# Optimization experiments

Hardware: AMD Instinct MI355X
Metric: run time of the kernel (lower is better)

Reference implementation:

```python
import jax, jax.numpy as jnp
import numpy as np

LOW_DIM, SKIP_DIM, OUT_DIM = 512, 256, 256
EPS_IDW = 1e-8
EPS_LN = 1e-5
K = 3


def setup_inputs() -> dict:
    key = jax.random.key(0)
    ks = jax.random.split(key, 10)
    B, N, S = 4, 8192, 2048
    xyz_hi = jax.random.uniform(ks[0], (B, N, 3), dtype=jnp.float32)
    xyz_lo = jax.random.uniform(ks[1], (B, S, 3), dtype=jnp.float32)
    feat_skip = jax.random.normal(ks[2], (B, N, SKIP_DIM), dtype=jnp.float32)
    feat_lo = jax.random.normal(ks[3], (B, S, LOW_DIM), dtype=jnp.float32)
    in_dim = LOW_DIM + SKIP_DIM
    W1 = jax.random.normal(ks[4], (in_dim, OUT_DIM), dtype=jnp.float32) / np.sqrt(in_dim)
    b1 = jnp.zeros((OUT_DIM,), dtype=jnp.float32)
    W2 = jax.random.normal(ks[5], (OUT_DIM, OUT_DIM), dtype=jnp.float32) / np.sqrt(OUT_DIM)
    b2 = jnp.zeros((OUT_DIM,), dtype=jnp.float32)
    gamma = jnp.ones((OUT_DIM,), dtype=jnp.float32)
    beta = jnp.zeros((OUT_DIM,), dtype=jnp.float32)
    return {"xyz_hi": xyz_hi, "xyz_lo": xyz_lo, "feat_skip": feat_skip,
            "feat_lo": feat_lo, "W1": W1, "b1": b1, "W2": W2, "b2": b2,
            "gamma": gamma, "beta": beta}


def _layer_norm(x, gamma, beta):
    mu = jnp.mean(x, axis=-1, keepdims=True)
    var = jnp.mean(jnp.square(x - mu), axis=-1, keepdims=True)
    return (x - mu) * jax.lax.rsqrt(var + EPS_LN) * gamma + beta


def reference(xyz_hi, xyz_lo, feat_skip, feat_lo, W1, b1, W2, b2, gamma, beta):
    B, N, _ = xyz_hi.shape
    _, S, _ = xyz_lo.shape
    if S == 1:
        interpolated = jnp.broadcast_to(feat_lo, (B, N, feat_lo.shape[-1]))
    else:
        # pairwise Euclidean distances: (B, N, S)
        d2 = (jnp.sum(xyz_hi ** 2, -1)[:, :, None]
              + jnp.sum(xyz_lo ** 2, -1)[:, None, :]
              - 2.0 * jnp.einsum('bnd,bsd->bns', xyz_hi, xyz_lo))
        dists = jnp.sqrt(jnp.maximum(d2, 0.0))
        # smallest-3 via top_k on negated distances
        neg_d, knn_idx = jax.lax.top_k(-dists, K)          # (B, N, 3)
        dk = -neg_d
        inv_d = 1.0 / (dk + EPS_IDW)
        weights = inv_d / jnp.sum(inv_d, axis=-1, keepdims=True)  # (B, N, 3)
        # gather neighbor features: (B, N, 3, low_dim)
        knn_feat = feat_lo[jnp.arange(B)[:, None, None], knn_idx]
        interpolated = jnp.einsum('bnk,bnkc->bnc', weights, knn_feat)
    fused = jnp.concatenate([feat_skip, interpolated], axis=-1)   # (B, N, skip+low)
    h = jax.nn.relu(fused @ W1 + b1)
    h = h @ W2 + b2
    return _layer_norm(h, gamma, beta)
```

## Files before the change

kernel.cpp:

```cpp
#include <hip/hip_runtime.h>
#include <hip/hip_bf16.h>
#include <stdint.h>

typedef unsigned short u16;
typedef __attribute__((ext_vector_type(8))) short short8;
typedef __attribute__((ext_vector_type(4))) float f32x4;

#define BB 4
#define NN 8192
#define SS 2048
#define MTOT 32768
#define CSKIP 256
#define CLO 512
#define CIN 768
#define COUT 256

__device__ __forceinline__ u16 f2bf(float f) {
  unsigned u = __float_as_uint(f);
  u += 0x7fffu + ((u >> 16) & 1u);
  return (u16)(u >> 16);
}

__device__ __forceinline__ void gl_lds16(const void* g, void* l) {
  __builtin_amdgcn_global_load_lds(
      (const __attribute__((address_space(1))) void*)g,
      (__attribute__((address_space(3))) void*)l, 16, 0, 0);
}

__global__ __launch_bounds__(256) void wconv_kernel(const float* __restrict__ W1,
                                                    const float* __restrict__ W2,
                                                    u16* __restrict__ W1T,
                                                    u16* __restrict__ W2T) {
  int i = blockIdx.x * 256 + threadIdx.x;
  if (i < CIN * COUT) {
    int n = i / CIN, k = i - n * CIN;
    W1T[i] = f2bf(W1[(size_t)k * COUT + n]);
  } else if (i < CIN * COUT + COUT * COUT) {
    int j = i - CIN * COUT;
    int n = j >> 8, k = j & 255;
    W2T[j] = f2bf(W2[(size_t)k * COUT + n]);
  }
}

__global__ __launch_bounds__(512) void knn_kernel(
    const float* __restrict__ xyz_hi, const float* __restrict__ xyz_lo,
    float* __restrict__ wq_g, int* __restrict__ iq_g) {
  __shared__ float4 sxyz[SS];
  __shared__ float md[8][64][3];
  __shared__ int   mi[8][64][3];

  int tid = threadIdx.x;
  int blk = blockIdx.x;
  int b = blk >> 7;
  const float* xl = xyz_lo + (size_t)b * SS * 3;
  for (int j = tid; j < SS; j += 512)
    sxyz[j] = make_float4(xl[j * 3 + 0], xl[j * 3 + 1], xl[j * 3 + 2], 0.f);
  __syncthreads();

  int wave = tid >> 6, lane = tid & 63;
  int qm = blk * 64 + lane;
  float qx = xyz_hi[(size_t)qm * 3 + 0];
  float qy = xyz_hi[(size_t)qm * 3 + 1];
  float qz = xyz_hi[(size_t)qm * 3 + 2];

  float b0 = 1e30f, b1 = 1e30f, b2 = 1e30f;
  int i0 = -1, i1 = -1, i2 = -1;
  int j0 = wave * 256;
#pragma unroll 4
  for (int jj = 0; jj < 256; ++jj) {
    int j = j0 + jj;
    float4 p = sxyz[j];
    float dx = p.x - qx, dy = p.y - qy, dz = p.z - qz;
    float d = fmaf(dx, dx, fmaf(dy, dy, dz * dz));
    bool c = d < b2;
    b2 = c ? d : b2; i2 = c ? j : i2;
    bool s = b2 < b1;
    float tb = b1; b1 = s ? b2 : b1; b2 = s ? tb : b2;
    int ti = i1;   i1 = s ? i2 : i1; i2 = s ? ti : i2;
    bool v = b1 < b0;
    float ub = b0; b0 = v ? b1 : b0; b1 = v ? ub : b1;
    int ui = i0;   i0 = v ? i1 : i0; i1 = v ? ui : i1;
  }
  md[wave][lane][0] = b0; mi[wave][lane][0] = i0;
  md[wave][lane][1] = b1; mi[wave][lane][1] = i1;
  md[wave][lane][2] = b2; mi[wave][lane][2] = i2;
  __syncthreads();

  if (tid < 64) {
    int q = tid;
    float fb0 = 1e30f, fb1 = 1e30f, fb2 = 1e30f;
    int fi0 = -1, fi1 = -1, fi2 = -1;
    for (int p = 0; p < 8; ++p)
#pragma unroll
      for (int s = 0; s < 3; ++s) {
        float d = md[p][q][s]; int ix = mi[p][q][s];
        if (d < fb2 || (d == fb2 && ix < fi2)) {
          fb2 = d; fi2 = ix;
          if (fb2 < fb1 || (fb2 == fb1 && fi2 < fi1)) {
            float t = fb1; fb1 = fb2; fb2 = t; int ti = fi1; fi1 = fi2; fi2 = ti;
          }
          if (fb1 < fb0 || (fb1 == fb0 && fi1 < fi0)) {
            float t = fb0; fb0 = fb1; fb1 = t; int ti = fi0; fi0 = fi1; fi1 = ti;
          }
        }
      }
    int qm2 = blk * 64 + q;
    float d0 = sqrtf(fb0), d1 = sqrtf(fb1), d2 = sqrtf(fb2);
    float inv0 = 1.0f / (d0 + 1e-8f);
    float inv1 = 1.0f / (d1 + 1e-8f);
    float inv2 = 1.0f / (d2 + 1e-8f);
    float s = inv0 + inv1 + inv2;
    wq_g[(size_t)qm2 * 3 + 0] = inv0 / s;
    wq_g[(size_t)qm2 * 3 + 1] = inv1 / s;
    wq_g[(size_t)qm2 * 3 + 2] = inv2 / s;
    iq_g[(size_t)qm2 * 3 + 0] = fi0;
    iq_g[(size_t)qm2 * 3 + 1] = fi1;
    iq_g[(size_t)qm2 * 3 + 2] = fi2;
  }
}

__global__ __launch_bounds__(256, 2) void gemm1_fused_kernel(
    const float* __restrict__ feat_skip, const float* __restrict__ feat_lo,
    const float* __restrict__ wq_g, const int* __restrict__ iq_g,
    const u16* __restrict__ W1T, const float* __restrict__ b1,
    u16* __restrict__ H) {
  __shared__ u16 As[64 * 72];
  __shared__ u16 Bs[256 * 64];
  int tid = threadIdx.x;
  int m0 = blockIdx.x << 6;
  int b = blockIdx.x >> 7;
  int w = tid >> 6, lane = tid & 63;
  int quad = lane >> 4, l16 = lane & 15;

  int srow = tid >> 2;
  int sc16 = (tid & 3) << 4;
  float w0 = wq_g[(size_t)(m0 + srow) * 3 + 0];
  float w1 = wq_g[(size_t)(m0 + srow) * 3 + 1];
  float w2 = wq_g[(size_t)(m0 + srow) * 3 + 2];
  int i0 = iq_g[(size_t)(m0 + srow) * 3 + 0];
  int i1 = iq_g[(size_t)(m0 + srow) * 3 + 1];
  int i2 = iq_g[(size_t)(m0 + srow) * 3 + 2];
  const float* fl0 = feat_lo + ((size_t)b * SS + i0) * CLO + sc16;
  const float* fl1 = feat_lo + ((size_t)b * SS + i1) * CLO + sc16;
  const float* fl2 = feat_lo + ((size_t)b * SS + i2) * CLO + sc16;
  const float* fsk = feat_skip + (size_t)(m0 + srow) * CSKIP + sc16;
  u16* As_dst = As + srow * 72 + sc16;

  f32x4 zero = {0.f, 0.f, 0.f, 0.f};
  f32x4 acc[4][4];
#pragma unroll
  for (int tm = 0; tm < 4; ++tm)
#pragma unroll
    for (int tn = 0; tn < 4; ++tn) acc[tm][tn] = zero;

  for (int kc = 0; kc < 12; ++kc) {
    __syncthreads();
#pragma unroll
    for (int r = 0; r < 8; ++r) {
      int u = tid + r * 256;
      int nrow = u >> 3, c = u & 7;
      int cg = c ^ (nrow & 7);
      gl_lds16(W1T + (size_t)nrow * CIN + kc * 64 + cg * 8, (char*)Bs + u * 16);
    }
    float av[16];
    if (kc < 4) {
      const float* p = fsk + kc * 64;
#pragma unroll
      for (int c = 0; c < 4; ++c) {
        float4 x = *(const float4*)(p + c * 4);
        av[4 * c + 0] = x.x; av[4 * c + 1] = x.y;
        av[4 * c + 2] = x.z; av[4 * c + 3] = x.w;
      }
    } else {
      int c0 = (kc - 4) * 64;
#pragma unroll
      for (int c = 0; c < 4; ++c) {
        float4 a = *(const float4*)(fl0 + c0 + c * 4);
        float4 d = *(const float4*)(fl1 + c0 + c * 4);
        float4 e = *(const float4*)(fl2 + c0 + c * 4);
        av[4 * c + 0] = fmaf(w0, a.x, fmaf(w1, d.x, w2 * e.x));
        av[4 * c + 1] = fmaf(w0, a.y, fmaf(w1, d.y, w2 * e.y));
        av[4 * c + 2] = fmaf(w0, a.z, fmaf(w1, d.z, w2 * e.z));
        av[4 * c + 3] = fmaf(w0, a.w, fmaf(w1, d.w, w2 * e.w));
      }
    }
    union { __hip_bfloat162 h2[8]; uint4 u4[2]; } pk;
#pragma unroll
    for (int c = 0; c < 8; ++c)
      pk.h2[c] = __float22bfloat162_rn(make_float2(av[2 * c], av[2 * c + 1]));
    *(uint4*)As_dst = pk.u4[0];
    *(uint4*)(As_dst + 8) = pk.u4[1];
    __syncthreads();

#pragma unroll
    for (int ko = 0; ko < 2; ++ko) {
      int ck = ko * 4 + quad;
      short8 af[4], bf[4];
#pragma unroll
      for (int t = 0; t < 4; ++t)
        af[t] = *(const short8*)(As + (t * 16 + l16) * 72 + ko * 32 + quad * 8);
#pragma unroll
      for (int t = 0; t < 4; ++t) {
        int rr = w * 64 + t * 16 + l16;
        bf[t] = *(const short8*)(Bs + (rr * 8 + (ck ^ (rr & 7))) * 8);
      }
#pragma unroll
      for (int tm = 0; tm < 4; ++tm)
#pragma unroll
        for (int tn = 0; tn < 4; ++tn)
          acc[tm][tn] = __builtin_amdgcn_mfma_f32_16x16x32_bf16(af[tm], bf[tn], acc[tm][tn], 0, 0, 0);
    }
  }

  float bias[4];
#pragma unroll
  for (int tn = 0; tn < 4; ++tn) bias[tn] = b1[w * 64 + tn * 16 + l16];
#pragma unroll
  for (int tm = 0; tm < 4; ++tm)
#pragma unroll
    for (int tn = 0; tn < 4; ++tn) {
      int col = w * 64 + tn * 16 + l16;
#pragma unroll
      for (int r = 0; r < 4; ++r) {
        int row = m0 + tm * 16 + quad * 4 + r;
        float v = acc[tm][tn][r] + bias[tn];
        v = v > 0.f ? v : 0.f;
        H[(size_t)row * COUT + col] = f2bf(v);
      }
    }
}

__global__ __launch_bounds__(256, 2) void gemm2_ln_kernel(const u16* __restrict__ H,
                                                          const u16* __restrict__ Bt,
                                                          const float* __restrict__ b2,
                                                          const float* __restrict__ gamma,
                                                          const float* __restrict__ beta,
                                                          float* __restrict__ out) {
  __shared__ u16 As[64 * 64];
  __shared__ u16 Bs[256 * 64];
  __shared__ float red[4][64][2];
  __shared__ float stats[64][2];
  int tid = threadIdx.x;
  int m0 = blockIdx.x << 6;
  int w = tid >> 6, lane = tid & 63;
  int quad = lane >> 4, l16 = lane & 15;

  f32x4 zero = {0.f, 0.f, 0.f, 0.f};
  f32x4 acc[4][4];
#pragma unroll
  for (int tm = 0; tm < 4; ++tm)
#pragma unroll
    for (int tn = 0; tn < 4; ++tn) acc[tm][tn] = zero;

  for (int kc = 0; kc < 4; ++kc) {
    __syncthreads();
#pragma unroll
    for (int r = 0; r < 2; ++r) {
      int u = tid + r * 256;
      int row = u >> 3, c = u & 7;
      int cg = c ^ (row & 7);
      gl_lds16(H + (size_t)(m0 + row) * COUT + kc * 64 + cg * 8, (char*)As + u * 16);
    }
#pragma unroll
    for (int r = 0; r < 8; ++r) {
      int u = tid + r * 256;
      int nrow = u >> 3, c = u & 7;
      int cg = c ^ (nrow & 7);
      gl_lds16(Bt + (size_t)nrow * COUT + kc * 64 + cg * 8, (char*)Bs + u * 16);
    }
    __syncthreads();

#pragma unroll
    for (int ko = 0; ko < 2; ++ko) {
      int ck = ko * 4 + quad;
      short8 af[4], bf[4];
#pragma unroll
      for (int t = 0; t < 4; ++t) {
        int ra = t * 16 + l16;
        af[t] = *(const short8*)(As + (ra * 8 + (ck ^ (ra & 7))) * 8);
      }
#pragma unroll
      for (int t = 0; t < 4; ++t) {
        int rr = w * 64 + t * 16 + l16;
        bf[t] = *(const short8*)(Bs + (rr * 8 + (ck ^ (rr & 7))) * 8);
      }
#pragma unroll
      for (int tm = 0; tm < 4; ++tm)
#pragma unroll
        for (int tn = 0; tn < 4; ++tn)
          acc[tm][tn] = __builtin_amdgcn_mfma_f32_16x16x32_bf16(af[tm], bf[tn], acc[tm][tn], 0, 0, 0);
    }
  }

  float bias[4], g[4], be[4];
#pragma unroll
  for (int tn = 0; tn < 4; ++tn) {
    int col = w * 64 + tn * 16 + l16;
    bias[tn] = b2[col]; g[tn] = gamma[col]; be[tn] = beta[col];
  }
#pragma unroll
  for (int tm = 0; tm < 4; ++tm)
#pragma unroll
    for (int r = 0; r < 4; ++r) {
      float s = 0.f, sq = 0.f;
#pragma unroll
      for (int tn = 0; tn < 4; ++tn) {
        float v = acc[tm][tn][r] + bias[tn];
        acc[tm][tn][r] = v;
        s += v; sq += v * v;
      }
#pragma unroll
      for (int msk = 1; msk < 16; msk <<= 1) {
        s += __shfl_xor(s, msk);
        sq += __shfl_xor(sq, msk);
      }
      if (l16 == 0) {
        int rl = tm * 16 + quad * 4 + r;
        red[w][rl][0] = s;
        red[w][rl][1] = sq;
      }
    }
  __syncthreads();
  if (tid < 64) {
    float s = red[0][tid][0] + red[1][tid][0] + red[2][tid][0] + red[3][tid][0];
    float sq = red[0][tid][1] + red[1][tid][1] + red[2][tid][1] + red[3][tid][1];
    float mu = s * (1.f / 256.f);
    float var = sq * (1.f / 256.f) - mu * mu;
    stats[tid][0] = mu;
    stats[tid][1] = rsqrtf(var + 1e-5f);
  }
  __syncthreads();
#pragma unroll
  for (int tm = 0; tm < 4; ++tm)
#pragma unroll
    for (int r = 0; r < 4; ++r) {
      int rl = tm * 16 + quad * 4 + r;
      float mu = stats[rl][0], rstd = stats[rl][1];
#pragma unroll
      for (int tn = 0; tn < 4; ++tn) {
        int col = w * 64 + tn * 16 + l16;
        out[(size_t)(m0 + rl) * COUT + col] = (acc[tm][tn][r] - mu) * rstd * g[tn] + be[tn];
      }
    }
}

extern "C" void kernel_launch(void* const* d_in, const int* in_sizes, int n_in,
                              void* d_out, int out_size, void* d_ws, size_t ws_size,
                              hipStream_t stream) {
  const float* xyz_hi    = (const float*)d_in[0];
  const float* xyz_lo    = (const float*)d_in[1];
  const float* feat_skip = (const float*)d_in[2];
  const float* feat_lo   = (const float*)d_in[3];
  const float* W1        = (const float*)d_in[4];
  const float* b1        = (const float*)d_in[5];
  const float* W2        = (const float*)d_in[6];
  const float* b2        = (const float*)d_in[7];
  const float* gamma     = (const float*)d_in[8];
  const float* beta      = (const float*)d_in[9];
  float* out = (float*)d_out;

  char* ws = (char*)d_ws;
  u16*   H    = (u16*)ws;
  u16*   W1T  = (u16*)(ws + 16777216);
  u16*   W2T  = (u16*)(ws + 16777216 + 393216);
  float* wq_g = (float*)(ws + 16777216 + 393216 + 131072);
  int*   iq_g = (int*)(ws + 16777216 + 393216 + 131072 + 393216);

  wconv_kernel<<<1024, 256, 0, stream>>>(W1, W2, W1T, W2T);
  knn_kernel<<<MTOT / 64, 512, 0, stream>>>(xyz_hi, xyz_lo, wq_g, iq_g);
  gemm1_fused_kernel<<<MTOT / 64, 256, 0, stream>>>(feat_skip, feat_lo, wq_g, iq_g, W1T, b1, H);
  gemm2_ln_kernel<<<MTOT / 64, 256, 0, stream>>>(H, W2T, b2, gamma, beta, out);
}
```

Baseline: 193.6 us.

## Project low-res features through W1 before interpolation to shrink GEMM1

```diff
diff --git a/kernel.cpp b/kernel.cpp
--- a/kernel.cpp
+++ b/kernel.cpp
@@ -29,14 +29,19 @@
 
 __global__ __launch_bounds__(256) void wconv_kernel(const float* __restrict__ W1,
                                                     const float* __restrict__ W2,
-                                                    u16* __restrict__ W1T,
+                                                    u16* __restrict__ W1aT,
+                                                    u16* __restrict__ W1bT,
                                                     u16* __restrict__ W2T) {
   int i = blockIdx.x * 256 + threadIdx.x;
-  if (i < CIN * COUT) {
-    int n = i / CIN, k = i - n * CIN;
-    W1T[i] = f2bf(W1[(size_t)k * COUT + n]);
-  } else if (i < CIN * COUT + COUT * COUT) {
-    int j = i - CIN * COUT;
+  if (i < 65536) {
+    int n = i >> 8, k = i & 255;
+    W1aT[i] = f2bf(W1[(size_t)k * COUT + n]);
+  } else if (i < 65536 + 131072) {
+    int j = i - 65536;
+    int n = j >> 9, k = j & 511;
+    W1bT[j] = f2bf(W1[(size_t)(256 + k) * COUT + n]);
+  } else {
+    int j = i - 65536 - 131072;
     int n = j >> 8, k = j & 255;
     W2T[j] = f2bf(W2[(size_t)k * COUT + n]);
   }
@@ -119,32 +124,95 @@
   }
 }
 
-__global__ __launch_bounds__(256, 2) void gemm1_fused_kernel(
-    const float* __restrict__ feat_skip, const float* __restrict__ feat_lo,
+__global__ __launch_bounds__(256, 4) void ggemm_kernel(
+    const float* __restrict__ feat_lo, const u16* __restrict__ W1bT,
+    float* __restrict__ G) {
+  __shared__ u16 As[32 * 40];
+  __shared__ u16 Bs[256 * 32];
+  int tid = threadIdx.x;
+  int m0 = blockIdx.x << 5;
+  int w = tid >> 6, lane = tid & 63;
+  int quad = lane >> 4, l16 = lane & 15;
+
+  int srow = tid >> 3, s4 = (tid & 7) << 2;
+  const float* arow = feat_lo + (size_t)(m0 + srow) * CLO + s4;
+  u16* As_dst = As + srow * 40 + s4;
+
+  f32x4 zero = {0.f, 0.f, 0.f, 0.f};
+  f32x4 acc[2][4];
+#pragma unroll
+  for (int tm = 0; tm < 2; ++tm)
+#pragma unroll
+    for (int tn = 0; tn < 4; ++tn) acc[tm][tn] = zero;
+
+  for (int kc = 0; kc < 16; ++kc) {
+    __syncthreads();
+#pragma unroll
+    for (int r = 0; r < 4; ++r) {
+      int u = tid + r * 256;
+      int nrow = u >> 2, c = u & 3;
+      int cg = c ^ (nrow & 3);
+      gl_lds16(W1bT + (size_t)nrow * CLO + kc * 32 + cg * 8, (char*)Bs + u * 16);
+    }
+    float4 av = *(const float4*)(arow + kc * 32);
+    union { __hip_bfloat162 h2[2]; uint2 u2; } pk;
+    pk.h2[0] = __float22bfloat162_rn(make_float2(av.x, av.y));
+    pk.h2[1] = __float22bfloat162_rn(make_float2(av.z, av.w));
+    *(uint2*)As_dst = pk.u2;
+    __syncthreads();
+
+    short8 af[2], bf[4];
+#pragma unroll
+    for (int t = 0; t < 2; ++t)
+      af[t] = *(const short8*)(As + (t * 16 + l16) * 40 + quad * 8);
+#pragma unroll
+    for (int t = 0; t < 4; ++t) {
+      int rr = w * 64 + t * 16 + l16;
+      bf[t] = *(const short8*)(Bs + (rr * 4 + (quad ^ (rr & 3))) * 8);
+    }
+#pragma unroll
+    for (int tm = 0; tm < 2; ++tm)
+#pragma unroll
+      for (int tn = 0; tn < 4; ++tn)
+        acc[tm][tn] = __builtin_amdgcn_mfma_f32_16x16x32_bf16(af[tm], bf[tn], acc[tm][tn], 0, 0, 0);
+  }
+
+#pragma unroll
+  for (int tm = 0; tm < 2; ++tm)
+#pragma unroll
+    for (int tn = 0; tn < 4; ++tn) {
+      int col = w * 64 + tn * 16 + l16;
+#pragma unroll
+      for (int r = 0; r < 4; ++r) {
+        int row = m0 + tm * 16 + quad * 4 + r;
+        G[(size_t)row * COUT + col] = acc[tm][tn][r];
+      }
+    }
+}
+
+__global__ __launch_bounds__(256, 2) void gemm1p_kernel(
+    const float* __restrict__ feat_skip, const u16* __restrict__ W1aT,
+    const float* __restrict__ b1, const float* __restrict__ G,
     const float* __restrict__ wq_g, const int* __restrict__ iq_g,
-    const u16* __restrict__ W1T, const float* __restrict__ b1,
     u16* __restrict__ H) {
-  __shared__ u16 As[64 * 72];
-  __shared__ u16 Bs[256 * 64];
+  __shared__ u16 As[64 * 40];
+  __shared__ u16 Bs[256 * 32];
+  __shared__ float swq[192];
+  __shared__ int   siq[192];
   int tid = threadIdx.x;
   int m0 = blockIdx.x << 6;
-  int b = blockIdx.x >> 7;
+  int bS = (m0 >> 13) * SS;
   int w = tid >> 6, lane = tid & 63;
   int quad = lane >> 4, l16 = lane & 15;
 
-  int srow = tid >> 2;
-  int sc16 = (tid & 3) << 4;
-  float w0 = wq_g[(size_t)(m0 + srow) * 3 + 0];
-  float w1 = wq_g[(size_t)(m0 + srow) * 3 + 1];
-  float w2 = wq_g[(size_t)(m0 + srow) * 3 + 2];
-  int i0 = iq_g[(size_t)(m0 + srow) * 3 + 0];
-  int i1 = iq_g[(size_t)(m0 + srow) * 3 + 1];
-  int i2 = iq_g[(size_t)(m0 + srow) * 3 + 2];
-  const float* fl0 = feat_lo + ((size_t)b * SS + i0) * CLO + sc16;
-  const float* fl1 = feat_lo + ((size_t)b * SS + i1) * CLO + sc16;
-  const float* fl2 = feat_lo + ((size_t)b * SS + i2) * CLO + sc16;
-  const float* fsk = feat_skip + (size_t)(m0 + srow) * CSKIP + sc16;
-  u16* As_dst = As + srow * 72 + sc16;
+  if (tid < 192) {
+    swq[tid] = wq_g[(size_t)m0 * 3 + tid];
+    siq[tid] = iq_g[(size_t)m0 * 3 + tid];
+  }
+
+  int srow = tid >> 2, sc8 = (tid & 3) << 3;
+  const float* arow = feat_skip + (size_t)(m0 + srow) * CSKIP + sc8;
+  u16* As_dst = As + srow * 40 + sc8;
 
   f32x4 zero = {0.f, 0.f, 0.f, 0.f};
   f32x4 acc[4][4];
@@ -153,79 +221,61 @@
 #pragma unroll
     for (int tn = 0; tn < 4; ++tn) acc[tm][tn] = zero;
 
-  for (int kc = 0; kc < 12; ++kc) {
-    __syncthreads();
-#pragma unroll
-    for (int r = 0; r < 8; ++r) {
+  for (int kc = 0; kc < 8; ++kc) {
+    __syncthreads();
+#pragma unroll
+    for (int r = 0; r < 4; ++r) {
       int u = tid + r * 256;
-      int nrow = u >> 3, c = u & 7;
-      int cg = c ^ (nrow & 7);
-      gl_lds16(W1T + (size_t)nrow * CIN + kc * 64 + cg * 8, (char*)Bs + u * 16);
-    }
-    float av[16];
-    if (kc < 4) {
-      const float* p = fsk + kc * 64;
-#pragma unroll
-      for (int c = 0; c < 4; ++c) {
-        float4 x = *(const float4*)(p + c * 4);
-        av[4 * c + 0] = x.x; av[4 * c + 1] = x.y;
-        av[4 * c + 2] = x.z; av[4 * c + 3] = x.w;
-      }
-    } else {
-      int c0 = (kc - 4) * 64;
-#pragma unroll
-      for (int c = 0; c < 4; ++c) {
-        float4 a = *(const float4*)(fl0 + c0 + c * 4);
-        float4 d = *(const float4*)(fl1 + c0 + c * 4);
-        float4 e = *(const float4*)(fl2 + c0 + c * 4);
-        av[4 * c + 0] = fmaf(w0, a.x, fmaf(w1, d.x, w2 * e.x));
-        av[4 * c + 1] = fmaf(w0, a.y, fmaf(w1, d.y, w2 * e.y));
-        av[4 * c + 2] = fmaf(w0, a.z, fmaf(w1, d.z, w2 * e.z));
-        av[4 * c + 3] = fmaf(w0, a.w, fmaf(w1, d.w, w2 * e.w));
-      }
-    }
-    union { __hip_bfloat162 h2[8]; uint4 u4[2]; } pk;
-#pragma unroll
-    for (int c = 0; c < 8; ++c)
-      pk.h2[c] = __float22bfloat162_rn(make_float2(av[2 * c], av[2 * c + 1]));
-    *(uint4*)As_dst = pk.u4[0];
-    *(uint4*)(As_dst + 8) = pk.u4[1];
-    __syncthreads();
-
-#pragma unroll
-    for (int ko = 0; ko < 2; ++ko) {
-      int ck = ko * 4 + quad;
-      short8 af[4], bf[4];
-#pragma unroll
-      for (int t = 0; t < 4; ++t)
-        af[t] = *(const short8*)(As + (t * 16 + l16) * 72 + ko * 32 + quad * 8);
-#pragma unroll
-      for (int t = 0; t < 4; ++t) {
-        int rr = w * 64 + t * 16 + l16;
-        bf[t] = *(const short8*)(Bs + (rr * 8 + (ck ^ (rr & 7))) * 8);
-      }
-#pragma unroll
-      for (int tm = 0; tm < 4; ++tm)
-#pragma unroll
-        for (int tn = 0; tn < 4; ++tn)
-          acc[tm][tn] = __builtin_amdgcn_mfma_f32_16x16x32_bf16(af[tm], bf[tn], acc[tm][tn], 0, 0, 0);
-    }
+      int nrow = u >> 2, c = u & 3;
+      int cg = c ^ (nrow & 3);
+      gl_lds16(W1aT + (size_t)nrow * CSKIP + kc * 32 + cg * 8, (char*)Bs + u * 16);
+    }
+    float4 x0 = *(const float4*)(arow + kc * 32);
+    float4 x1 = *(const float4*)(arow + kc * 32 + 4);
+    union { __hip_bfloat162 h2[4]; uint4 u4; } pk;
+    pk.h2[0] = __float22bfloat162_rn(make_float2(x0.x, x0.y));
+    pk.h2[1] = __float22bfloat162_rn(make_float2(x0.z, x0.w));
+    pk.h2[2] = __float22bfloat162_rn(make_float2(x1.x, x1.y));
+    pk.h2[3] = __float22bfloat162_rn(make_float2(x1.z, x1.w));
+    *(uint4*)As_dst = pk.u4;
+    __syncthreads();
+
+    short8 af[4], bf[4];
+#pragma unroll
+    for (int t = 0; t < 4; ++t)
+      af[t] = *(const short8*)(As + (t * 16 + l16) * 40 + quad * 8);
+#pragma unroll
+    for (int t = 0; t < 4; ++t) {
+      int rr = w * 64 + t * 16 + l16;
+      bf[t] = *(const short8*)(Bs + (rr * 4 + (quad ^ (rr & 3))) * 8);
+    }
+#pragma unroll
+    for (int tm = 0; tm < 4; ++tm)
+#pragma unroll
+      for (int tn = 0; tn < 4; ++tn)
+        acc[tm][tn] = __builtin_amdgcn_mfma_f32_16x16x32_bf16(af[tm], bf[tn], acc[tm][tn], 0, 0, 0);
   }
 
   float bias[4];
 #pragma unroll
   for (int tn = 0; tn < 4; ++tn) bias[tn] = b1[w * 64 + tn * 16 + l16];
+
 #pragma unroll
   for (int tm = 0; tm < 4; ++tm)
 #pragma unroll
-    for (int tn = 0; tn < 4; ++tn) {
-      int col = w * 64 + tn * 16 + l16;
-#pragma unroll
-      for (int r = 0; r < 4; ++r) {
-        int row = m0 + tm * 16 + quad * 4 + r;
-        float v = acc[tm][tn][r] + bias[tn];
+    for (int r = 0; r < 4; ++r) {
+      int rl = tm * 16 + quad * 4 + r;
+      float w0 = swq[rl * 3 + 0], w1 = swq[rl * 3 + 1], w2 = swq[rl * 3 + 2];
+      const float* g0 = G + (size_t)(bS + siq[rl * 3 + 0]) * COUT;
+      const float* g1 = G + (size_t)(bS + siq[rl * 3 + 1]) * COUT;
+      const float* g2 = G + (size_t)(bS + siq[rl * 3 + 2]) * COUT;
+#pragma unroll
+      for (int tn = 0; tn < 4; ++tn) {
+        int col = w * 64 + tn * 16 + l16;
+        float gv = fmaf(w0, g0[col], fmaf(w1, g1[col], w2 * g2[col]));
+        float v = acc[tm][tn][r] + bias[tn] + gv;
         v = v > 0.f ? v : 0.f;
-        H[(size_t)row * COUT + col] = f2bf(v);
+        H[(size_t)(m0 + rl) * COUT + col] = f2bf(v);
       }
     }
 }
@@ -360,14 +410,17 @@
   float* out = (float*)d_out;
 
   char* ws = (char*)d_ws;
-  u16*   H    = (u16*)ws;
-  u16*   W1T  = (u16*)(ws + 16777216);
-  u16*   W2T  = (u16*)(ws + 16777216 + 393216);
-  float* wq_g = (float*)(ws + 16777216 + 393216 + 131072);
-  int*   iq_g = (int*)(ws + 16777216 + 393216 + 131072 + 393216);
-
-  wconv_kernel<<<1024, 256, 0, stream>>>(W1, W2, W1T, W2T);
+  u16*   H     = (u16*)ws;
+  u16*   W1aT  = (u16*)(ws + 16777216);
+  u16*   W1bT  = (u16*)(ws + 16908288);
+  u16*   W2T   = (u16*)(ws + 17170432);
+  float* wq_g  = (float*)(ws + 17301504);
+  int*   iq_g  = (int*)(ws + 17694720);
+  float* G     = (float*)(ws + 18087936);
+
+  wconv_kernel<<<1024, 256, 0, stream>>>(W1, W2, W1aT, W1bT, W2T);
   knn_kernel<<<MTOT / 64, 512, 0, stream>>>(xyz_hi, xyz_lo, wq_g, iq_g);
-  gemm1_fused_kernel<<<MTOT / 64, 256, 0, stream>>>(feat_skip, feat_lo, wq_g, iq_g, W1T, b1, H);
+  ggemm_kernel<<<(BB * SS) / 32, 256, 0, stream>>>(feat_lo, W1bT, G);
+  gemm1p_kernel<<<MTOT / 64, 256, 0, stream>>>(feat_skip, W1aT, b1, G, wq_g, iq_g, H);
   gemm2_ln_kernel<<<MTOT / 64, 256, 0, stream>>>(H, W2T, b2, gamma, beta, out);
 }
```

Result: no change. 190.4 us (-1.7%).
